# Kernel tuning notes

Hardware: AMD Instinct MI355X
Metric: run time of the kernel (lower is better)

Reference implementation:

```python
import jax, jax.numpy as jnp
import numpy as np

NEG_SLOPE = 0.2  # PyG HypergraphConv default negative_slope
HEADS, F_OUT = 4, 64


def setup_inputs() -> dict:
    key = jax.random.key(0)
    ks = jax.random.split(key, 8)
    N, E, NNZ, C_IN, C_OUT = 50000, 10000, 600000, 128, 64
    x = jax.random.normal(ks[0], (N, C_IN), jnp.float32)
    node = jax.random.randint(ks[1], (NNZ,), 0, N, jnp.int32)
    hedge = jax.random.randint(ks[2], (NNZ,), 0, E, jnp.int32)
    hedge = hedge.at[0].set(E - 1)  # ensure num_edges = max(hedge)+1 = E
    edge_index = jnp.stack([node, hedge])  # [2, NNZ]
    hyperedge_attr = jax.random.normal(ks[3], (E, C_IN), jnp.float32)  # init_hedge='rand'
    W1 = jax.random.normal(ks[4], (C_IN, HEADS * F_OUT), jnp.float32) / np.sqrt(C_IN)
    att1 = jax.random.normal(ks[5], (1, HEADS, 2 * F_OUT), jnp.float32) * 0.1
    b1 = jnp.zeros((HEADS * F_OUT,), jnp.float32)
    W2 = jax.random.normal(ks[6], (HEADS * F_OUT, C_OUT), jnp.float32) / np.sqrt(HEADS * F_OUT)
    b2 = jnp.zeros((C_OUT,), jnp.float32)
    return {"x": x, "edge_index": edge_index, "hyperedge_attr": hyperedge_attr,
            "W1": W1, "att1": att1, "b1": b1, "W2": W2, "b2": b2}


def _segment_softmax(logits, seg, num_segments):
    # PyG softmax: subtract per-segment max, exp, normalize with +1e-16
    m = jax.ops.segment_max(logits, seg, num_segments=num_segments)
    m = jnp.where(jnp.isfinite(m), m, 0.0)
    ex = jnp.exp(logits - m[seg])
    s = jax.ops.segment_sum(ex, seg, num_segments=num_segments)
    return ex / (s[seg] + 1e-16)


def _hconv(x, node, hedge, W, b, heads, f_out, num_edges, att=None, hyperedge_attr=None):
    """Faithful PyG HypergraphConv (attention_mode='node', concat=True)."""
    N = x.shape[0]
    E = num_edges
    nnz = node.shape[0]
    xh = (x @ W).reshape(N, heads, f_out)  # lin (bias-free) + view
    alpha = None
    if att is not None:
        he = (hyperedge_attr @ W).reshape(E, heads, f_out)
        # cat([x_i, x_j], -1) * att summed == split att into two halves
        alpha = (xh[node] * att[:, :, :f_out]).sum(-1) + (he[hedge] * att[:, :, f_out:]).sum(-1)
        alpha = jax.nn.leaky_relu(alpha, NEG_SLOPE)
        alpha = _segment_softmax(alpha, hedge, E)  # softmax per hyperedge ('node' mode)
    ones = jnp.ones((nnz,), x.dtype)
    D = jax.ops.segment_sum(ones, node, num_segments=N)  # node degrees (unit hyperedge weights)
    D = jnp.where(D > 0, 1.0 / D, 0.0)
    B = jax.ops.segment_sum(ones, hedge, num_segments=E)  # hyperedge sizes
    B = jnp.where(B > 0, 1.0 / B, 0.0)
    # propagate 1: nodes -> hyperedges (norm = B at target hyperedge)
    msg = B[hedge][:, None, None] * xh[node]
    if alpha is not None:
        msg = alpha[:, :, None] * msg
    eh = jax.ops.segment_sum(msg, hedge, num_segments=E)  # [E, H, F]
    # propagate 2: hyperedges -> nodes (norm = D at target node)
    msg2 = D[node][:, None, None] * eh[hedge]
    if alpha is not None:
        msg2 = alpha[:, :, None] * msg2
    out = jax.ops.segment_sum(msg2, node, num_segments=N)  # [N, H, F]
    return out.reshape(N, heads * f_out) + b


def reference(x, edge_index, hyperedge_attr, W1, att1, b1, W2, b2):
    node, hedge = edge_index[0], edge_index[1]
    E = hyperedge_attr.shape[0]  # num_edges = max(edge_index[1]) + 1 by construction
    h = _hconv(x, node, hedge, W1, b1, HEADS, F_OUT, E, att=att1, hyperedge_attr=hyperedge_attr)
    h = jax.nn.elu(h)  # dropout p=0 / eval mode -> identity
    out = _hconv(h, node, hedge, W2, b2, 1, W2.shape[1], E)  # last conv: no attention, heads=1
    return out
```

## Files before the change

### kernel.cpp

```cpp
#include <hip/hip_runtime.h>
#include <math.h>

#define LRELU_SLOPE 0.2f

static __device__ __forceinline__ float lrelu(float x) {
  return x >= 0.f ? x : LRELU_SLOPE * x;
}


__global__ void count_kernel(const int* __restrict__ node, const int* __restrict__ hedge,
                             int nnz, int* __restrict__ cnt_n, int* __restrict__ cnt_e) {
  int i = blockIdx.x * blockDim.x + threadIdx.x;
  if (i < nnz) {
    atomicAdd(&cnt_n[node[i]], 1);
    atomicAdd(&cnt_e[hedge[i]], 1);
  }
}

__global__ void recip_kernel(const int* __restrict__ cnt, float* __restrict__ rec, int n) {
  int i = blockIdx.x * blockDim.x + threadIdx.x;
  if (i < n) { int c = cnt[i]; rec[i] = c > 0 ? 1.f / (float)c : 0.f; }
}

__global__ __launch_bounds__(256) void scan1_kernel(const int* __restrict__ cnt,
                                                    int* __restrict__ off,
                                                    int* __restrict__ bsum, int n) {
  int b = blockIdx.x, tid = threadIdx.x, lane = tid & 63, wid = tid >> 6;
  int i0 = b * 1024 + tid * 4;
  int v0 = (i0 + 0 < n) ? cnt[i0 + 0] : 0;
  int v1 = (i0 + 1 < n) ? cnt[i0 + 1] : 0;
  int v2 = (i0 + 2 < n) ? cnt[i0 + 2] : 0;
  int v3 = (i0 + 3 < n) ? cnt[i0 + 3] : 0;
  int s = v0 + v1 + v2 + v3;
  int incl = s;
  #pragma unroll
  for (int d = 1; d < 64; d <<= 1) {
    int t = __shfl_up(incl, d);
    if (lane >= d) incl += t;
  }
  __shared__ int ws[4];
  if (lane == 63) ws[wid] = incl;
  __syncthreads();
  int woff = 0;
  #pragma unroll
  for (int w = 0; w < 4; ++w)
    if (w < wid) woff += ws[w];
  int run = woff + incl - s;
  if (i0 + 0 < n) off[i0 + 0] = run; run += v0;
  if (i0 + 1 < n) off[i0 + 1] = run; run += v1;
  if (i0 + 2 < n) off[i0 + 2] = run; run += v2;
  if (i0 + 3 < n) off[i0 + 3] = run;
  if (tid == 0) bsum[b] = ws[0] + ws[1] + ws[2] + ws[3];
}

__global__ void scan2_kernel(int* __restrict__ bsum, int nb) {
  int tid = threadIdx.x;
  int v = (tid < nb) ? bsum[tid] : 0;
  int incl = v;
  #pragma unroll
  for (int d = 1; d < 64; d <<= 1) {
    int t = __shfl_up(incl, d);
    if (tid >= d) incl += t;
  }
  if (tid < nb) bsum[tid] = incl - v;
  if (tid == 63) bsum[64] = incl;
}

__global__ void scan3_kernel(int* __restrict__ off, const int* __restrict__ bsum,
                             int n, int* __restrict__ cur) {
  int i = blockIdx.x * blockDim.x + threadIdx.x;
  if (i < n) {
    int v = off[i] + bsum[i >> 10];
    off[i] = v;
    cur[i] = v;
  }
  if (i == n) off[n] = bsum[64];
}

__global__ void scatter_kernel(const int* __restrict__ node, const int* __restrict__ hedge,
                               int nnz, int* __restrict__ cur_n, int* __restrict__ cur_e,
                               int* __restrict__ n_hedge, int* __restrict__ e_node) {
  int i = blockIdx.x * blockDim.x + threadIdx.x;
  if (i < nnz) {
    int nd = node[i], he = hedge[i];
    e_node[atomicAdd(&cur_e[he], 1)] = nd;
    n_hedge[atomicAdd(&cur_n[nd], 1)] = he;
  }
}


__global__ __launch_bounds__(256) void gemm1_kernel(
    const float* __restrict__ X, const float* __restrict__ W,
    float* __restrict__ Y, int R,
    const float* __restrict__ att, int half, float* __restrict__ adot) {
  __shared__ float xt[32][128];
  int r0 = blockIdx.x * 32;
  int tid = threadIdx.x, lane = tid & 63;
  int c0 = tid & 127, rh = tid >> 7;
  for (int i = tid; i < 32 * 32; i += 256) {
    int r = i >> 5, k4 = i & 31;
    int rr = r0 + r;
    float4 v = make_float4(0.f, 0.f, 0.f, 0.f);
    if (rr < R) v = reinterpret_cast<const float4*>(X)[(size_t)rr * 32 + k4];
    reinterpret_cast<float4*>(&xt[r][0])[k4] = v;
  }
  __syncthreads();
  float accA[16], accB[16];
  #pragma unroll
  for (int r = 0; r < 16; ++r) { accA[r] = 0.f; accB[r] = 0.f; }
  for (int k = 0; k < 128; k += 4) {
    float4 xv[16];
    #pragma unroll
    for (int r = 0; r < 16; ++r)
      xv[r] = *reinterpret_cast<const float4*>(&xt[rh * 16 + r][k]);
    #pragma unroll
    for (int kk = 0; kk < 4; ++kk) {
      float wa = W[(k + kk) * 256 + c0];
      float wb = W[(k + kk) * 256 + c0 + 128];
      #pragma unroll
      for (int r = 0; r < 16; ++r) {
        float xr = (kk == 0) ? xv[r].x : (kk == 1) ? xv[r].y : (kk == 2) ? xv[r].z : xv[r].w;
        accA[r] = fmaf(xr, wa, accA[r]);
        accB[r] = fmaf(xr, wb, accB[r]);
      }
    }
  }
  if (Y != nullptr) {
    #pragma unroll
    for (int r = 0; r < 16; ++r) {
      int rr = r0 + rh * 16 + r;
      if (rr < R) {
        Y[(size_t)rr * 256 + c0] = accA[r];
        Y[(size_t)rr * 256 + c0 + 128] = accB[r];
      }
    }
  }
  int hA = c0 >> 6;
  float avA = att[hA * 128 + half + lane];
  float avB = att[(hA + 2) * 128 + half + lane];
  #pragma unroll
  for (int r = 0; r < 16; ++r) {
    int rr = r0 + rh * 16 + r;
    float pA = accA[r] * avA;
    float pB = accB[r] * avB;
    #pragma unroll
    for (int s = 32; s >= 1; s >>= 1) {
      pA += __shfl_xor(pA, s);
      pB += __shfl_xor(pB, s);
    }
    if (lane == 0 && rr < R) {
      adot[rr * 4 + hA] = pA;
      adot[rr * 4 + hA + 2] = pB;
    }
  }
}


__global__ __launch_bounds__(256) void gemm2_kernel(const float* __restrict__ H,
                                                    const float* __restrict__ W,
                                                    float* __restrict__ Y, int R) {
  __shared__ float xt[32][256];
  int r0 = blockIdx.x * 32;
  int tid = threadIdx.x, c = tid & 63, rq = tid >> 6;
  for (int i = tid; i < 32 * 64; i += 256) {
    int r = i >> 6, k4 = i & 63;
    int rr = r0 + r;
    float4 v = make_float4(0.f, 0.f, 0.f, 0.f);
    if (rr < R) v = reinterpret_cast<const float4*>(H)[(size_t)rr * 64 + k4];
    reinterpret_cast<float4*>(&xt[r][0])[k4] = v;
  }
  __syncthreads();
  float acc[8];
  #pragma unroll
  for (int r = 0; r < 8; ++r) acc[r] = 0.f;
  for (int k = 0; k < 256; k += 4) {
    float4 xv[8];
    #pragma unroll
    for (int r = 0; r < 8; ++r)
      xv[r] = *reinterpret_cast<const float4*>(&xt[rq * 8 + r][k]);
    #pragma unroll
    for (int kk = 0; kk < 4; ++kk) {
      float w = W[(k + kk) * 64 + c];
      #pragma unroll
      for (int r = 0; r < 8; ++r) {
        float xr = (kk == 0) ? xv[r].x : (kk == 1) ? xv[r].y : (kk == 2) ? xv[r].z : xv[r].w;
        acc[r] = fmaf(xr, w, acc[r]);
      }
    }
  }
  #pragma unroll
  for (int r = 0; r < 8; ++r) {
    int rr = r0 + rq * 8 + r;
    if (rr < R) Y[(size_t)rr * 64 + c] = acc[r];
  }
}


__global__ __launch_bounds__(256) void p1_kernel(
    const int* __restrict__ off_e, const int* __restrict__ e_node,
    const float* __restrict__ xh, const float* __restrict__ a_n,
    const float* __restrict__ a_e, const float* __restrict__ Brec,
    float* __restrict__ eh, float4* __restrict__ pk, int E) {
  int tid = threadIdx.x, lane = tid & 63, wid = tid >> 6;
  int e = blockIdx.x * 4 + wid;
  if (e >= E) return;
  int beg = off_e[e], end = off_e[e + 1];
  int mm = lane & 15, h = lane >> 4, hsel = lane & 48;
  float aeh = a_e[e * 4 + h];

  float mx = -INFINITY;
  for (int base = beg; base < end; base += 16) {
    int m = base + mm;
    if (m < end) mx = fmaxf(mx, lrelu(a_n[e_node[m] * 4 + h] + aeh));
  }
  mx = fmaxf(mx, __shfl_xor(mx, 1));
  mx = fmaxf(mx, __shfl_xor(mx, 2));
  mx = fmaxf(mx, __shfl_xor(mx, 4));
  mx = fmaxf(mx, __shfl_xor(mx, 8));
  if (isinf(mx)) mx = 0.f;

  float4 acc = make_float4(0.f, 0.f, 0.f, 0.f);
  float ls = 0.f;
  for (int base = beg; base < end; base += 16) {
    int m = base + mm;
    int nd = 0;
    float w = 0.f;
    if (m < end) {
      nd = e_node[m];
      w = expf(lrelu(a_n[nd * 4 + h] + aeh) - mx);
      ls += w;
    }
    int cmax = min(16, end - base);
    for (int j = 0; j < cmax; ++j) {
      int ndj = __shfl(nd, j);
      float wj = __shfl(w, j | hsel);
      float4 v = reinterpret_cast<const float4*>(xh)[(size_t)ndj * 64 + lane];
      acc.x = fmaf(wj, v.x, acc.x);
      acc.y = fmaf(wj, v.y, acc.y);
      acc.z = fmaf(wj, v.z, acc.z);
      acc.w = fmaf(wj, v.w, acc.w);
    }
  }
  ls += __shfl_xor(ls, 1);
  ls += __shfl_xor(ls, 2);
  ls += __shfl_xor(ls, 4);
  ls += __shfl_xor(ls, 8);
  float rds = 1.f / (ls + 1e-16f);
  float sc = Brec[e] * rds;
  float4 o = make_float4(acc.x * sc, acc.y * sc, acc.z * sc, acc.w * sc);
  reinterpret_cast<float4*>(eh)[(size_t)e * 64 + lane] = o;
  if (mm == 0) pk[e * 4 + h] = make_float4(aeh, mx, rds, 0.f);
}

__global__ __launch_bounds__(256) void p2_kernel(
    const int* __restrict__ off_n, const int* __restrict__ n_hedge,
    const float* __restrict__ eh, const float* __restrict__ a_n,
    const float4* __restrict__ pk, const float* __restrict__ Drec,
    const float* __restrict__ b1, float* __restrict__ hout, int N) {
  int tid = threadIdx.x, lane = tid & 63, wid = tid >> 6;
  int n = blockIdx.x * 4 + wid;
  if (n >= N) return;
  int beg = off_n[n], end = off_n[n + 1];
  int mm = lane & 15, h = lane >> 4, hsel = lane & 48;
  float anh = a_n[n * 4 + h];

  float4 acc = make_float4(0.f, 0.f, 0.f, 0.f);
  for (int base = beg; base < end; base += 16) {
    int m = base + mm;
    int he = 0;
    float w = 0.f;
    if (m < end) {
      he = n_hedge[m];
      float4 p = pk[he * 4 + h];
      w = expf(lrelu(anh + p.x) - p.y) * p.z;
    }
    int cmax = min(16, end - base);
    for (int j = 0; j < cmax; ++j) {
      int hej = __shfl(he, j);
      float wj = __shfl(w, j | hsel);
      float4 v = reinterpret_cast<const float4*>(eh)[(size_t)hej * 64 + lane];
      acc.x = fmaf(wj, v.x, acc.x);
      acc.y = fmaf(wj, v.y, acc.y);
      acc.z = fmaf(wj, v.z, acc.z);
      acc.w = fmaf(wj, v.w, acc.w);
    }
  }
  float dr = Drec[n];
  float4 bb = reinterpret_cast<const float4*>(b1)[lane];
  float vx = fmaf(acc.x, dr, bb.x);
  float vy = fmaf(acc.y, dr, bb.y);
  float vz = fmaf(acc.z, dr, bb.z);
  float vw = fmaf(acc.w, dr, bb.w);
  float4 o;
  o.x = vx > 0.f ? vx : expm1f(vx);
  o.y = vy > 0.f ? vy : expm1f(vy);
  o.z = vz > 0.f ? vz : expm1f(vz);
  o.w = vw > 0.f ? vw : expm1f(vw);
  reinterpret_cast<float4*>(hout)[(size_t)n * 64 + lane] = o;
}


__global__ __launch_bounds__(256) void p1b_kernel(
    const int* __restrict__ off_e, const int* __restrict__ e_node,
    const float* __restrict__ xh2, const float* __restrict__ Brec,
    float* __restrict__ eh2, int E) {
  int tid = threadIdx.x, lane = tid & 63, wid = tid >> 6;
  int e = blockIdx.x * 4 + wid;
  if (e >= E) return;
  int f4 = lane & 15, mo = lane >> 4;
  int beg = off_e[e], end = off_e[e + 1];
  float4 acc = make_float4(0.f, 0.f, 0.f, 0.f);
  for (int m = beg + mo; m < end; m += 4) {
    float4 v = reinterpret_cast<const float4*>(xh2)[(size_t)e_node[m] * 16 + f4];
    acc.x += v.x; acc.y += v.y; acc.z += v.z; acc.w += v.w;
  }
  acc.x += __shfl_xor(acc.x, 16); acc.x += __shfl_xor(acc.x, 32);
  acc.y += __shfl_xor(acc.y, 16); acc.y += __shfl_xor(acc.y, 32);
  acc.z += __shfl_xor(acc.z, 16); acc.z += __shfl_xor(acc.z, 32);
  acc.w += __shfl_xor(acc.w, 16); acc.w += __shfl_xor(acc.w, 32);
  if (mo == 0) {
    float sc = Brec[e];
    float4 o = make_float4(acc.x * sc, acc.y * sc, acc.z * sc, acc.w * sc);
    reinterpret_cast<float4*>(eh2)[(size_t)e * 16 + f4] = o;
  }
}

__global__ __launch_bounds__(256) void p2b_kernel(
    const int* __restrict__ off_n, const int* __restrict__ n_hedge,
    const float* __restrict__ eh2, const float* __restrict__ Drec,
    const float* __restrict__ b2, float* __restrict__ out, int N) {
  int tid = threadIdx.x, lane = tid & 63, wid = tid >> 6;
  int n = blockIdx.x * 4 + wid;
  if (n >= N) return;
  int f4 = lane & 15, mo = lane >> 4;
  int beg = off_n[n], end = off_n[n + 1];
  float4 acc = make_float4(0.f, 0.f, 0.f, 0.f);
  for (int m = beg + mo; m < end; m += 4) {
    float4 v = reinterpret_cast<const float4*>(eh2)[(size_t)n_hedge[m] * 16 + f4];
    acc.x += v.x; acc.y += v.y; acc.z += v.z; acc.w += v.w;
  }
  acc.x += __shfl_xor(acc.x, 16); acc.x += __shfl_xor(acc.x, 32);
  acc.y += __shfl_xor(acc.y, 16); acc.y += __shfl_xor(acc.y, 32);
  acc.z += __shfl_xor(acc.z, 16); acc.z += __shfl_xor(acc.z, 32);
  acc.w += __shfl_xor(acc.w, 16); acc.w += __shfl_xor(acc.w, 32);
  if (mo == 0) {
    float dr = Drec[n];
    float4 bb = reinterpret_cast<const float4*>(b2)[f4];
    float4 o = make_float4(fmaf(acc.x, dr, bb.x), fmaf(acc.y, dr, bb.y),
                           fmaf(acc.z, dr, bb.z), fmaf(acc.w, dr, bb.w));
    reinterpret_cast<float4*>(out)[(size_t)n * 16 + f4] = o;
  }
}


extern "C" void kernel_launch(void* const* d_in, const int* in_sizes, int n_in,
                              void* d_out, int out_size, void* d_ws, size_t ws_size,
                              hipStream_t stream) {
  const float* x   = (const float*)d_in[0];
  const int*   ei  = (const int*)d_in[1];
  const float* hea = (const float*)d_in[2];
  const float* W1  = (const float*)d_in[3];
  const float* att = (const float*)d_in[4];
  const float* b1  = (const float*)d_in[5];
  const float* W2  = (const float*)d_in[6];
  const float* b2  = (const float*)d_in[7];

  const int C2  = in_sizes[7];
  const int CH  = in_sizes[6] / C2;
  const int CIN = in_sizes[3] / CH;
  const int N   = in_sizes[0] / CIN;
  const int E   = in_sizes[2] / CIN;
  const int NNZ = in_sizes[1] / 2;
  const int* node  = ei;
  const int* hedge = ei + NNZ;

  char* wp = (char*)d_ws;
  auto alloc = [&](size_t bytes) -> void* {
    void* p = (void*)wp;
    wp += (bytes + 255) & ~(size_t)255;
    return p;
  };
  float*  xh     = (float*) alloc((size_t)N * CH * 4);
  float*  eh     = (float*) alloc((size_t)E * CH * 4);
  float*  a_n    = (float*) alloc((size_t)N * 4 * 4);
  float*  a_e    = (float*) alloc((size_t)E * 4 * 4);
  float4* pk     = (float4*)alloc((size_t)E * 4 * 16);
  float*  Brec   = (float*) alloc((size_t)E * 4);
  float*  Drec   = (float*) alloc((size_t)N * 4);
  int*    cnt_e  = (int*)   alloc((size_t)E * 4);
  int*    cnt_n  = (int*)   alloc((size_t)N * 4);
  int*    off_e  = (int*)   alloc((size_t)(E + 1) * 4);
  int*    off_n  = (int*)   alloc((size_t)(N + 1) * 4);
  int*    cur_e  = (int*)   alloc((size_t)E * 4);
  int*    cur_n  = (int*)   alloc((size_t)N * 4);
  int*    e_node  = (int*)  alloc((size_t)NNZ * 4);
  int*    n_hedge = (int*)  alloc((size_t)NNZ * 4);
  float*  xh2    = (float*) alloc((size_t)N * C2 * 4);
  float*  eh2    = (float*) alloc((size_t)E * C2 * 4);
  int*    bsum_e = (int*)   alloc(65 * 4);
  int*    bsum_n = (int*)   alloc(65 * 4);
  float*  hact   = xh;

  hipMemsetAsync(cnt_e, 0, (size_t)E * 4, stream);
  hipMemsetAsync(cnt_n, 0, (size_t)N * 4, stream);

  const int tpb = 256;
  count_kernel<<<(NNZ + tpb - 1) / tpb, tpb, 0, stream>>>(node, hedge, NNZ, cnt_n, cnt_e);

  int nbE = (E + 1023) / 1024, nbN = (N + 1023) / 1024;
  scan1_kernel<<<nbE, 256, 0, stream>>>(cnt_e, off_e, bsum_e, E);
  scan2_kernel<<<1, 64, 0, stream>>>(bsum_e, nbE);
  scan3_kernel<<<(E + 1 + 255) / 256, 256, 0, stream>>>(off_e, bsum_e, E, cur_e);
  scan1_kernel<<<nbN, 256, 0, stream>>>(cnt_n, off_n, bsum_n, N);
  scan2_kernel<<<1, 64, 0, stream>>>(bsum_n, nbN);
  scan3_kernel<<<(N + 1 + 255) / 256, 256, 0, stream>>>(off_n, bsum_n, N, cur_n);

  recip_kernel<<<(E + tpb - 1) / tpb, tpb, 0, stream>>>(cnt_e, Brec, E);
  recip_kernel<<<(N + tpb - 1) / tpb, tpb, 0, stream>>>(cnt_n, Drec, N);
  scatter_kernel<<<(NNZ + tpb - 1) / tpb, tpb, 0, stream>>>(node, hedge, NNZ,
                                                            cur_n, cur_e, n_hedge, e_node);

  gemm1_kernel<<<(N + 31) / 32, 256, 0, stream>>>(x, W1, xh, N, att, 0, a_n);
  gemm1_kernel<<<(E + 31) / 32, 256, 0, stream>>>(hea, W1, nullptr, E, att, 64, a_e);

  p1_kernel<<<(E + 3) / 4, 256, 0, stream>>>(off_e, e_node, xh, a_n, a_e, Brec, eh, pk, E);
  p2_kernel<<<(N + 3) / 4, 256, 0, stream>>>(off_n, n_hedge, eh, a_n, pk, Drec, b1, hact, N);

  gemm2_kernel<<<(N + 31) / 32, 256, 0, stream>>>(hact, W2, xh2, N);
  p1b_kernel<<<(E + 3) / 4, 256, 0, stream>>>(off_e, e_node, xh2, Brec, eh2, E);
  p2b_kernel<<<(N + 3) / 4, 256, 0, stream>>>(off_n, n_hedge, eh2, Drec, b2, (float*)d_out, N);
}
```

Measured before the change: 603.9 us.

## Store intermediate features in bf16 and precompute per-incidence attention weights

Node and hyperedge feature intermediates (xh, eh, hact, xh2) are now packed as bf16 pairs instead of fp32, roughly halving gather traffic in the propagation kernels. The scatter kernel records each incidence's position in the node-major order, so p1 can write unnormalized attention weights into a per-incidence buffer. The softmax normalization is folded into eh, and p2 then reads alpha directly instead of recomputing exp per edge. The gather loops are restructured to load 8 rows at a time with two accumulators, and the small recip and scan2 launches are merged. This trades fp32 accuracy for bandwidth and adds an NNZ*4 float alpha buffer plus the npos array.

```diff
diff --git a/kernel.cpp b/kernel.cpp
--- a/kernel.cpp
+++ b/kernel.cpp
@@ -1,10 +1,24 @@
 #include <hip/hip_runtime.h>
 #include <math.h>
 
+typedef unsigned int u32;
+
 #define LRELU_SLOPE 0.2f
 
 static __device__ __forceinline__ float lrelu(float x) {
   return x >= 0.f ? x : LRELU_SLOPE * x;
+}
+static __device__ __forceinline__ float bflo(u32 u) {
+  return __builtin_bit_cast(float, u << 16);
+}
+static __device__ __forceinline__ float bfhi(u32 u) {
+  return __builtin_bit_cast(float, u & 0xFFFF0000u);
+}
+static __device__ __forceinline__ u32 f2bf_pack(float a, float b) {
+  u32 ua = __builtin_bit_cast(u32, a), ub = __builtin_bit_cast(u32, b);
+  ua = (ua + 0x7FFFu + ((ua >> 16) & 1u)) >> 16;
+  ub = (ub + 0x7FFFu + ((ub >> 16) & 1u)) & 0xFFFF0000u;
+  return ua | ub;
 }
 
 
@@ -17,20 +31,20 @@
   }
 }
 
-__global__ void recip_kernel(const int* __restrict__ cnt, float* __restrict__ rec, int n) {
-  int i = blockIdx.x * blockDim.x + threadIdx.x;
-  if (i < n) { int c = cnt[i]; rec[i] = c > 0 ? 1.f / (float)c : 0.f; }
-}
-
 __global__ __launch_bounds__(256) void scan1_kernel(const int* __restrict__ cnt,
                                                     int* __restrict__ off,
-                                                    int* __restrict__ bsum, int n) {
+                                                    int* __restrict__ bsum,
+                                                    float* __restrict__ rec, int n) {
   int b = blockIdx.x, tid = threadIdx.x, lane = tid & 63, wid = tid >> 6;
   int i0 = b * 1024 + tid * 4;
   int v0 = (i0 + 0 < n) ? cnt[i0 + 0] : 0;
   int v1 = (i0 + 1 < n) ? cnt[i0 + 1] : 0;
   int v2 = (i0 + 2 < n) ? cnt[i0 + 2] : 0;
   int v3 = (i0 + 3 < n) ? cnt[i0 + 3] : 0;
+  if (i0 + 0 < n) rec[i0 + 0] = v0 > 0 ? 1.f / (float)v0 : 0.f;
+  if (i0 + 1 < n) rec[i0 + 1] = v1 > 0 ? 1.f / (float)v1 : 0.f;
+  if (i0 + 2 < n) rec[i0 + 2] = v2 > 0 ? 1.f / (float)v2 : 0.f;
+  if (i0 + 3 < n) rec[i0 + 3] = v3 > 0 ? 1.f / (float)v3 : 0.f;
   int s = v0 + v1 + v2 + v3;
   int incl = s;
   #pragma unroll
@@ -53,17 +67,20 @@
   if (tid == 0) bsum[b] = ws[0] + ws[1] + ws[2] + ws[3];
 }
 
-__global__ void scan2_kernel(int* __restrict__ bsum, int nb) {
+__global__ void scan2_kernel(int* __restrict__ bsum_e, int nbe,
+                             int* __restrict__ bsum_n, int nbn) {
+  int* b = blockIdx.x == 0 ? bsum_e : bsum_n;
+  int nb = blockIdx.x == 0 ? nbe : nbn;
   int tid = threadIdx.x;
-  int v = (tid < nb) ? bsum[tid] : 0;
+  int v = (tid < nb) ? b[tid] : 0;
   int incl = v;
   #pragma unroll
   for (int d = 1; d < 64; d <<= 1) {
     int t = __shfl_up(incl, d);
     if (tid >= d) incl += t;
   }
-  if (tid < nb) bsum[tid] = incl - v;
-  if (tid == 63) bsum[64] = incl;
+  if (tid < nb) b[tid] = incl - v;
+  if (tid == 63) b[64] = incl;
 }
 
 __global__ void scan3_kernel(int* __restrict__ off, const int* __restrict__ bsum,
@@ -79,29 +96,32 @@
 
 __global__ void scatter_kernel(const int* __restrict__ node, const int* __restrict__ hedge,
                                int nnz, int* __restrict__ cur_n, int* __restrict__ cur_e,
-                               int* __restrict__ n_hedge, int* __restrict__ e_node) {
+                               int* __restrict__ n_hedge, int* __restrict__ e_node,
+                               int* __restrict__ npos) {
   int i = blockIdx.x * blockDim.x + threadIdx.x;
   if (i < nnz) {
     int nd = node[i], he = hedge[i];
-    e_node[atomicAdd(&cur_e[he], 1)] = nd;
-    n_hedge[atomicAdd(&cur_n[nd], 1)] = he;
+    int pe = atomicAdd(&cur_e[he], 1);
+    int pn = atomicAdd(&cur_n[nd], 1);
+    e_node[pe] = nd;
+    n_hedge[pn] = he;
+    npos[pe] = pn;
   }
 }
 
 
 __global__ __launch_bounds__(256) void gemm1_kernel(
     const float* __restrict__ X, const float* __restrict__ W,
-    float* __restrict__ Y, int R,
+    u32* __restrict__ Yb, int R,
     const float* __restrict__ att, int half, float* __restrict__ adot) {
   __shared__ float xt[32][128];
-  int r0 = blockIdx.x * 32;
-  int tid = threadIdx.x, lane = tid & 63;
-  int c0 = tid & 127, rh = tid >> 7;
+  int r0 = blockIdx.x * 32, tid = threadIdx.x, lane = tid & 63;
+  int c = tid & 127, rh = tid >> 7;
   for (int i = tid; i < 32 * 32; i += 256) {
     int r = i >> 5, k4 = i & 31;
     int rr = r0 + r;
-    float4 v = make_float4(0.f, 0.f, 0.f, 0.f);
-    if (rr < R) v = reinterpret_cast<const float4*>(X)[(size_t)rr * 32 + k4];
+    float4 v = rr < R ? reinterpret_cast<const float4*>(X)[(size_t)rr * 32 + k4]
+                      : make_float4(0.f, 0.f, 0.f, 0.f);
     reinterpret_cast<float4*>(&xt[r][0])[k4] = v;
   }
   __syncthreads();
@@ -115,8 +135,8 @@
       xv[r] = *reinterpret_cast<const float4*>(&xt[rh * 16 + r][k]);
     #pragma unroll
     for (int kk = 0; kk < 4; ++kk) {
-      float wa = W[(k + kk) * 256 + c0];
-      float wb = W[(k + kk) * 256 + c0 + 128];
+      float wa = W[(k + kk) * 256 + 2 * c];
+      float wb = W[(k + kk) * 256 + 2 * c + 1];
       #pragma unroll
       for (int r = 0; r < 16; ++r) {
         float xr = (kk == 0) ? xv[r].x : (kk == 1) ? xv[r].y : (kk == 2) ? xv[r].z : xv[r].w;
@@ -125,203 +145,274 @@
       }
     }
   }
-  if (Y != nullptr) {
+  if (Yb != nullptr) {
     #pragma unroll
     for (int r = 0; r < 16; ++r) {
       int rr = r0 + rh * 16 + r;
-      if (rr < R) {
-        Y[(size_t)rr * 256 + c0] = accA[r];
-        Y[(size_t)rr * 256 + c0 + 128] = accB[r];
-      }
-    }
-  }
-  int hA = c0 >> 6;
-  float avA = att[hA * 128 + half + lane];
-  float avB = att[(hA + 2) * 128 + half + lane];
+      if (rr < R) Yb[(size_t)rr * 128 + c] = f2bf_pack(accA[r], accB[r]);
+    }
+  }
+  int hh = c >> 5, cl = c & 31;
+  float avA = att[hh * 128 + half + 2 * cl];
+  float avB = att[hh * 128 + half + 2 * cl + 1];
   #pragma unroll
   for (int r = 0; r < 16; ++r) {
+    float p = fmaf(accA[r], avA, accB[r] * avB);
+    #pragma unroll
+    for (int s = 16; s >= 1; s >>= 1) p += __shfl_xor(p, s);
     int rr = r0 + rh * 16 + r;
-    float pA = accA[r] * avA;
-    float pB = accB[r] * avB;
-    #pragma unroll
-    for (int s = 32; s >= 1; s >>= 1) {
-      pA += __shfl_xor(pA, s);
-      pB += __shfl_xor(pB, s);
-    }
-    if (lane == 0 && rr < R) {
-      adot[rr * 4 + hA] = pA;
-      adot[rr * 4 + hA + 2] = pB;
-    }
-  }
-}
-
-
-__global__ __launch_bounds__(256) void gemm2_kernel(const float* __restrict__ H,
-                                                    const float* __restrict__ W,
-                                                    float* __restrict__ Y, int R) {
-  __shared__ float xt[32][256];
-  int r0 = blockIdx.x * 32;
-  int tid = threadIdx.x, c = tid & 63, rq = tid >> 6;
-  for (int i = tid; i < 32 * 64; i += 256) {
-    int r = i >> 6, k4 = i & 63;
+    if ((lane & 31) == 0 && rr < R) adot[rr * 4 + hh] = p;
+  }
+}
+
+
+__global__ __launch_bounds__(256) void gemm2_kernel(
+    const u32* __restrict__ Hb, const float* __restrict__ W,
+    u32* __restrict__ Yb, int R) {
+  __shared__ u32 ht[32][128];
+  int r0 = blockIdx.x * 32, tid = threadIdx.x;
+  int cp = tid & 31, rg = tid >> 5;
+  for (int i = tid; i < 32 * 32; i += 256) {
+    int r = i >> 5, q = i & 31;
     int rr = r0 + r;
-    float4 v = make_float4(0.f, 0.f, 0.f, 0.f);
-    if (rr < R) v = reinterpret_cast<const float4*>(H)[(size_t)rr * 64 + k4];
-    reinterpret_cast<float4*>(&xt[r][0])[k4] = v;
+    uint4 v = rr < R ? reinterpret_cast<const uint4*>(Hb)[(size_t)rr * 32 + q]
+                     : make_uint4(0u, 0u, 0u, 0u);
+    reinterpret_cast<uint4*>(&ht[r][0])[q] = v;
   }
   __syncthreads();
-  float acc[8];
+  float acc[4][2] = {};
+  for (int k = 0; k < 256; k += 4) {
+    float w0a = W[(k + 0) * 64 + 2 * cp], w0b = W[(k + 0) * 64 + 2 * cp + 1];
+    float w1a = W[(k + 1) * 64 + 2 * cp], w1b = W[(k + 1) * 64 + 2 * cp + 1];
+    float w2a = W[(k + 2) * 64 + 2 * cp], w2b = W[(k + 2) * 64 + 2 * cp + 1];
+    float w3a = W[(k + 3) * 64 + 2 * cp], w3b = W[(k + 3) * 64 + 2 * cp + 1];
+    #pragma unroll
+    for (int r = 0; r < 4; ++r) {
+      uint2 u = *reinterpret_cast<const uint2*>(&ht[rg * 4 + r][k >> 1]);
+      float x0 = bflo(u.x), x1 = bfhi(u.x), x2 = bflo(u.y), x3 = bfhi(u.y);
+      acc[r][0] = fmaf(x0, w0a, acc[r][0]); acc[r][1] = fmaf(x0, w0b, acc[r][1]);
+      acc[r][0] = fmaf(x1, w1a, acc[r][0]); acc[r][1] = fmaf(x1, w1b, acc[r][1]);
+      acc[r][0] = fmaf(x2, w2a, acc[r][0]); acc[r][1] = fmaf(x2, w2b, acc[r][1]);
+      acc[r][0] = fmaf(x3, w3a, acc[r][0]); acc[r][1] = fmaf(x3, w3b, acc[r][1]);
+    }
+  }
   #pragma unroll
-  for (int r = 0; r < 8; ++r) acc[r] = 0.f;
-  for (int k = 0; k < 256; k += 4) {
-    float4 xv[8];
-    #pragma unroll
-    for (int r = 0; r < 8; ++r)
-      xv[r] = *reinterpret_cast<const float4*>(&xt[rq * 8 + r][k]);
-    #pragma unroll
-    for (int kk = 0; kk < 4; ++kk) {
-      float w = W[(k + kk) * 64 + c];
-      #pragma unroll
-      for (int r = 0; r < 8; ++r) {
-        float xr = (kk == 0) ? xv[r].x : (kk == 1) ? xv[r].y : (kk == 2) ? xv[r].z : xv[r].w;
-        acc[r] = fmaf(xr, w, acc[r]);
-      }
-    }
-  }
-  #pragma unroll
-  for (int r = 0; r < 8; ++r) {
-    int rr = r0 + rq * 8 + r;
-    if (rr < R) Y[(size_t)rr * 64 + c] = acc[r];
+  for (int r = 0; r < 4; ++r) {
+    int rr = r0 + rg * 4 + r;
+    if (rr < R) Yb[(size_t)rr * 32 + cp] = f2bf_pack(acc[r][0], acc[r][1]);
   }
 }
 
 
 __global__ __launch_bounds__(256) void p1_kernel(
     const int* __restrict__ off_e, const int* __restrict__ e_node,
-    const float* __restrict__ xh, const float* __restrict__ a_n,
-    const float* __restrict__ a_e, const float* __restrict__ Brec,
-    float* __restrict__ eh, float4* __restrict__ pk, int E) {
-  int tid = threadIdx.x, lane = tid & 63, wid = tid >> 6;
+    const int* __restrict__ npos, const u32* __restrict__ xhb,
+    const float* __restrict__ a_n, const float* __restrict__ a_e,
+    const float* __restrict__ Brec, float* __restrict__ alpha_n,
+    u32* __restrict__ ehb, int E) {
+  int tid = threadIdx.x, lane = tid & 63;
+  int wid = __builtin_amdgcn_readfirstlane(tid >> 6);
   int e = blockIdx.x * 4 + wid;
   if (e >= E) return;
   int beg = off_e[e], end = off_e[e + 1];
-  int mm = lane & 15, h = lane >> 4, hsel = lane & 48;
+  int h = lane >> 4;
+  bool h0 = (lane & 15) == 0;
   float aeh = a_e[e * 4 + h];
 
   float mx = -INFINITY;
-  for (int base = beg; base < end; base += 16) {
-    int m = base + mm;
-    if (m < end) mx = fmaxf(mx, lrelu(a_n[e_node[m] * 4 + h] + aeh));
-  }
-  mx = fmaxf(mx, __shfl_xor(mx, 1));
-  mx = fmaxf(mx, __shfl_xor(mx, 2));
-  mx = fmaxf(mx, __shfl_xor(mx, 4));
-  mx = fmaxf(mx, __shfl_xor(mx, 8));
+  {
+    int m = beg;
+    for (; m + 8 <= end; m += 8) {
+      float l[8];
+      #pragma unroll
+      for (int i = 0; i < 8; ++i) {
+        int nd = e_node[m + i];
+        l[i] = lrelu(a_n[nd * 4 + h] + aeh);
+      }
+      #pragma unroll
+      for (int i = 0; i < 8; ++i) mx = fmaxf(mx, l[i]);
+    }
+    if (m < end) {
+      int last = end - 1;
+      #pragma unroll
+      for (int i = 0; i < 8; ++i) {
+        int mm = m + i, mc = mm < last ? mm : last;
+        int nd = e_node[mc];
+        mx = fmaxf(mx, lrelu(a_n[nd * 4 + h] + aeh));
+      }
+    }
+  }
   if (isinf(mx)) mx = 0.f;
 
-  float4 acc = make_float4(0.f, 0.f, 0.f, 0.f);
+  const uint2* rows = reinterpret_cast<const uint2*>(xhb);
+  float4 A = make_float4(0.f, 0.f, 0.f, 0.f), B = A;
   float ls = 0.f;
-  for (int base = beg; base < end; base += 16) {
-    int m = base + mm;
-    int nd = 0;
-    float w = 0.f;
-    if (m < end) {
-      nd = e_node[m];
-      w = expf(lrelu(a_n[nd * 4 + h] + aeh) - mx);
-      ls += w;
-    }
-    int cmax = min(16, end - base);
-    for (int j = 0; j < cmax; ++j) {
-      int ndj = __shfl(nd, j);
-      float wj = __shfl(w, j | hsel);
-      float4 v = reinterpret_cast<const float4*>(xh)[(size_t)ndj * 64 + lane];
-      acc.x = fmaf(wj, v.x, acc.x);
-      acc.y = fmaf(wj, v.y, acc.y);
-      acc.z = fmaf(wj, v.z, acc.z);
-      acc.w = fmaf(wj, v.w, acc.w);
-    }
-  }
-  ls += __shfl_xor(ls, 1);
-  ls += __shfl_xor(ls, 2);
-  ls += __shfl_xor(ls, 4);
-  ls += __shfl_xor(ls, 8);
+  int m = beg;
+  for (; m + 8 <= end; m += 8) {
+    int ns[8]; float wsv[8];
+    #pragma unroll
+    for (int i = 0; i < 8; ++i) {
+      ns[i] = e_node[m + i];
+      wsv[i] = expf(lrelu(a_n[ns[i] * 4 + h] + aeh) - mx);
+      ls += wsv[i];
+      if (h0) alpha_n[npos[m + i] * 4 + h] = wsv[i];
+    }
+    uint2 vs[8];
+    #pragma unroll
+    for (int i = 0; i < 8; ++i) vs[i] = rows[(size_t)ns[i] * 64 + lane];
+    #pragma unroll
+    for (int i = 0; i < 8; ++i) {
+      float4& C = (i & 1) ? B : A;
+      C.x = fmaf(wsv[i], bflo(vs[i].x), C.x);
+      C.y = fmaf(wsv[i], bfhi(vs[i].x), C.y);
+      C.z = fmaf(wsv[i], bflo(vs[i].y), C.z);
+      C.w = fmaf(wsv[i], bfhi(vs[i].y), C.w);
+    }
+  }
+  if (m < end) {
+    int last = end - 1;
+    int ns[8]; float wsv[8];
+    #pragma unroll
+    for (int i = 0; i < 8; ++i) {
+      int mm = m + i, mc = mm < last ? mm : last;
+      ns[i] = e_node[mc];
+      float w = expf(lrelu(a_n[ns[i] * 4 + h] + aeh) - mx);
+      bool v = mm < end;
+      wsv[i] = v ? w : 0.f;
+      ls += wsv[i];
+      if (v && h0) alpha_n[npos[mc] * 4 + h] = w;
+    }
+    uint2 vs[8];
+    #pragma unroll
+    for (int i = 0; i < 8; ++i) vs[i] = rows[(size_t)ns[i] * 64 + lane];
+    #pragma unroll
+    for (int i = 0; i < 8; ++i) {
+      float4& C = (i & 1) ? B : A;
+      C.x = fmaf(wsv[i], bflo(vs[i].x), C.x);
+      C.y = fmaf(wsv[i], bfhi(vs[i].x), C.y);
+      C.z = fmaf(wsv[i], bflo(vs[i].y), C.z);
+      C.w = fmaf(wsv[i], bfhi(vs[i].y), C.w);
+    }
+  }
   float rds = 1.f / (ls + 1e-16f);
-  float sc = Brec[e] * rds;
-  float4 o = make_float4(acc.x * sc, acc.y * sc, acc.z * sc, acc.w * sc);
-  reinterpret_cast<float4*>(eh)[(size_t)e * 64 + lane] = o;
-  if (mm == 0) pk[e * 4 + h] = make_float4(aeh, mx, rds, 0.f);
-}
+  float sc = (Brec[e] * rds) * rds;
+  uint2 st;
+  st.x = f2bf_pack((A.x + B.x) * sc, (A.y + B.y) * sc);
+  st.y = f2bf_pack((A.z + B.z) * sc, (A.w + B.w) * sc);
+  reinterpret_cast<uint2*>(ehb)[(size_t)e * 64 + lane] = st;
+}
+
 
 __global__ __launch_bounds__(256) void p2_kernel(
     const int* __restrict__ off_n, const int* __restrict__ n_hedge,
-    const float* __restrict__ eh, const float* __restrict__ a_n,
-    const float4* __restrict__ pk, const float* __restrict__ Drec,
-    const float* __restrict__ b1, float* __restrict__ hout, int N) {
-  int tid = threadIdx.x, lane = tid & 63, wid = tid >> 6;
+    const u32* __restrict__ ehb, const float* __restrict__ alpha_n,
+    const float* __restrict__ Drec, const float* __restrict__ b1,
+    u32* __restrict__ hactb, int N) {
+  int tid = threadIdx.x, lane = tid & 63;
+  int wid = __builtin_amdgcn_readfirstlane(tid >> 6);
   int n = blockIdx.x * 4 + wid;
   if (n >= N) return;
   int beg = off_n[n], end = off_n[n + 1];
-  int mm = lane & 15, h = lane >> 4, hsel = lane & 48;
-  float anh = a_n[n * 4 + h];
-
-  float4 acc = make_float4(0.f, 0.f, 0.f, 0.f);
-  for (int base = beg; base < end; base += 16) {
-    int m = base + mm;
-    int he = 0;
-    float w = 0.f;
-    if (m < end) {
-      he = n_hedge[m];
-      float4 p = pk[he * 4 + h];
-      w = expf(lrelu(anh + p.x) - p.y) * p.z;
-    }
-    int cmax = min(16, end - base);
-    for (int j = 0; j < cmax; ++j) {
-      int hej = __shfl(he, j);
-      float wj = __shfl(w, j | hsel);
-      float4 v = reinterpret_cast<const float4*>(eh)[(size_t)hej * 64 + lane];
-      acc.x = fmaf(wj, v.x, acc.x);
-      acc.y = fmaf(wj, v.y, acc.y);
-      acc.z = fmaf(wj, v.z, acc.z);
-      acc.w = fmaf(wj, v.w, acc.w);
+  int h = lane >> 4;
+  const uint2* rows = reinterpret_cast<const uint2*>(ehb);
+  float4 A = make_float4(0.f, 0.f, 0.f, 0.f), B = A;
+  int m = beg;
+  for (; m + 8 <= end; m += 8) {
+    int es[8]; float wsv[8];
+    #pragma unroll
+    for (int i = 0; i < 8; ++i) {
+      es[i] = n_hedge[m + i];
+      wsv[i] = alpha_n[(m + i) * 4 + h];
+    }
+    uint2 vs[8];
+    #pragma unroll
+    for (int i = 0; i < 8; ++i) vs[i] = rows[(size_t)es[i] * 64 + lane];
+    #pragma unroll
+    for (int i = 0; i < 8; ++i) {
+      float4& C = (i & 1) ? B : A;
+      C.x = fmaf(wsv[i], bflo(vs[i].x), C.x);
+      C.y = fmaf(wsv[i], bfhi(vs[i].x), C.y);
+      C.z = fmaf(wsv[i], bflo(vs[i].y), C.z);
+      C.w = fmaf(wsv[i], bfhi(vs[i].y), C.w);
+    }
+  }
+  if (m < end) {
+    int last = end - 1;
+    int es[8]; float wsv[8];
+    #pragma unroll
+    for (int i = 0; i < 8; ++i) {
+      int mm = m + i, mc = mm < last ? mm : last;
+      es[i] = n_hedge[mc];
+      wsv[i] = (mm < end) ? alpha_n[mc * 4 + h] : 0.f;
+    }
+    uint2 vs[8];
+    #pragma unroll
+    for (int i = 0; i < 8; ++i) vs[i] = rows[(size_t)es[i] * 64 + lane];
+    #pragma unroll
+    for (int i = 0; i < 8; ++i) {
+      float4& C = (i & 1) ? B : A;
+      C.x = fmaf(wsv[i], bflo(vs[i].x), C.x);
+      C.y = fmaf(wsv[i], bfhi(vs[i].x), C.y);
+      C.z = fmaf(wsv[i], bflo(vs[i].y), C.z);
+      C.w = fmaf(wsv[i], bfhi(vs[i].y), C.w);
     }
   }
   float dr = Drec[n];
   float4 bb = reinterpret_cast<const float4*>(b1)[lane];
-  float vx = fmaf(acc.x, dr, bb.x);
-  float vy = fmaf(acc.y, dr, bb.y);
-  float vz = fmaf(acc.z, dr, bb.z);
-  float vw = fmaf(acc.w, dr, bb.w);
-  float4 o;
-  o.x = vx > 0.f ? vx : expm1f(vx);
-  o.y = vy > 0.f ? vy : expm1f(vy);
-  o.z = vz > 0.f ? vz : expm1f(vz);
-  o.w = vw > 0.f ? vw : expm1f(vw);
-  reinterpret_cast<float4*>(hout)[(size_t)n * 64 + lane] = o;
+  float vx = fmaf(A.x + B.x, dr, bb.x);
+  float vy = fmaf(A.y + B.y, dr, bb.y);
+  float vz = fmaf(A.z + B.z, dr, bb.z);
+  float vw = fmaf(A.w + B.w, dr, bb.w);
+  vx = vx > 0.f ? vx : expm1f(vx);
+  vy = vy > 0.f ? vy : expm1f(vy);
+  vz = vz > 0.f ? vz : expm1f(vz);
+  vw = vw > 0.f ? vw : expm1f(vw);
+  uint2 st;
+  st.x = f2bf_pack(vx, vy);
+  st.y = f2bf_pack(vz, vw);
+  reinterpret_cast<uint2*>(hactb)[(size_t)n * 64 + lane] = st;
 }
 
 
 __global__ __launch_bounds__(256) void p1b_kernel(
     const int* __restrict__ off_e, const int* __restrict__ e_node,
-    const float* __restrict__ xh2, const float* __restrict__ Brec,
+    const u32* __restrict__ xh2b, const float* __restrict__ Brec,
     float* __restrict__ eh2, int E) {
-  int tid = threadIdx.x, lane = tid & 63, wid = tid >> 6;
+  int tid = threadIdx.x, lane = tid & 63;
+  int wid = __builtin_amdgcn_readfirstlane(tid >> 6);
   int e = blockIdx.x * 4 + wid;
   if (e >= E) return;
-  int f4 = lane & 15, mo = lane >> 4;
+  int f8 = lane & 15, mo = lane >> 4;
   int beg = off_e[e], end = off_e[e + 1];
-  float4 acc = make_float4(0.f, 0.f, 0.f, 0.f);
-  for (int m = beg + mo; m < end; m += 4) {
-    float4 v = reinterpret_cast<const float4*>(xh2)[(size_t)e_node[m] * 16 + f4];
-    acc.x += v.x; acc.y += v.y; acc.z += v.z; acc.w += v.w;
-  }
-  acc.x += __shfl_xor(acc.x, 16); acc.x += __shfl_xor(acc.x, 32);
-  acc.y += __shfl_xor(acc.y, 16); acc.y += __shfl_xor(acc.y, 32);
-  acc.z += __shfl_xor(acc.z, 16); acc.z += __shfl_xor(acc.z, 32);
-  acc.w += __shfl_xor(acc.w, 16); acc.w += __shfl_xor(acc.w, 32);
+  const uint2* rows = reinterpret_cast<const uint2*>(xh2b);
+  float4 A = make_float4(0.f, 0.f, 0.f, 0.f), B = A;
+  int m = beg;
+  for (; m + 8 <= end; m += 8) {
+    int n0 = e_node[m + mo], n1 = e_node[m + 4 + mo];
+    uint2 u0 = rows[(size_t)n0 * 16 + f8];
+    uint2 u1 = rows[(size_t)n1 * 16 + f8];
+    A.x += bflo(u0.x); A.y += bfhi(u0.x); A.z += bflo(u0.y); A.w += bfhi(u0.y);
+    B.x += bflo(u1.x); B.y += bfhi(u1.x); B.z += bflo(u1.y); B.w += bfhi(u1.y);
+  }
+  if (m < end) {
+    int last = end - 1;
+    int mm0 = m + mo, mm1 = m + 4 + mo;
+    int mc0 = mm0 < last ? mm0 : last, mc1 = mm1 < last ? mm1 : last;
+    int n0 = e_node[mc0], n1 = e_node[mc1];
+    uint2 u0 = rows[(size_t)n0 * 16 + f8];
+    uint2 u1 = rows[(size_t)n1 * 16 + f8];
+    if (mm0 < end) { A.x += bflo(u0.x); A.y += bfhi(u0.x); A.z += bflo(u0.y); A.w += bfhi(u0.y); }
+    if (mm1 < end) { B.x += bflo(u1.x); B.y += bfhi(u1.x); B.z += bflo(u1.y); B.w += bfhi(u1.y); }
+  }
+  A.x += B.x; A.y += B.y; A.z += B.z; A.w += B.w;
+  A.x += __shfl_xor(A.x, 16); A.x += __shfl_xor(A.x, 32);
+  A.y += __shfl_xor(A.y, 16); A.y += __shfl_xor(A.y, 32);
+  A.z += __shfl_xor(A.z, 16); A.z += __shfl_xor(A.z, 32);
+  A.w += __shfl_xor(A.w, 16); A.w += __shfl_xor(A.w, 32);
   if (mo == 0) {
     float sc = Brec[e];
-    float4 o = make_float4(acc.x * sc, acc.y * sc, acc.z * sc, acc.w * sc);
-    reinterpret_cast<float4*>(eh2)[(size_t)e * 16 + f4] = o;
+    float4 o = make_float4(A.x * sc, A.y * sc, A.z * sc, A.w * sc);
+    reinterpret_cast<float4*>(eh2)[(size_t)e * 16 + f8] = o;
   }
 }
 
@@ -329,26 +420,43 @@
     const int* __restrict__ off_n, const int* __restrict__ n_hedge,
     const float* __restrict__ eh2, const float* __restrict__ Drec,
     const float* __restrict__ b2, float* __restrict__ out, int N) {
-  int tid = threadIdx.x, lane = tid & 63, wid = tid >> 6;
+  int tid = threadIdx.x, lane = tid & 63;
+  int wid = __builtin_amdgcn_readfirstlane(tid >> 6);
   int n = blockIdx.x * 4 + wid;
   if (n >= N) return;
-  int f4 = lane & 15, mo = lane >> 4;
+  int f8 = lane & 15, mo = lane >> 4;
   int beg = off_n[n], end = off_n[n + 1];
-  float4 acc = make_float4(0.f, 0.f, 0.f, 0.f);
-  for (int m = beg + mo; m < end; m += 4) {
-    float4 v = reinterpret_cast<const float4*>(eh2)[(size_t)n_hedge[m] * 16 + f4];
-    acc.x += v.x; acc.y += v.y; acc.z += v.z; acc.w += v.w;
-  }
-  acc.x += __shfl_xor(acc.x, 16); acc.x += __shfl_xor(acc.x, 32);
-  acc.y += __shfl_xor(acc.y, 16); acc.y += __shfl_xor(acc.y, 32);
-  acc.z += __shfl_xor(acc.z, 16); acc.z += __shfl_xor(acc.z, 32);
-  acc.w += __shfl_xor(acc.w, 16); acc.w += __shfl_xor(acc.w, 32);
+  const float4* rows = reinterpret_cast<const float4*>(eh2);
+  float4 A = make_float4(0.f, 0.f, 0.f, 0.f), B = A;
+  int m = beg;
+  for (; m + 8 <= end; m += 8) {
+    int e0 = n_hedge[m + mo], e1 = n_hedge[m + 4 + mo];
+    float4 v0 = rows[(size_t)e0 * 16 + f8];
+    float4 v1 = rows[(size_t)e1 * 16 + f8];
+    A.x += v0.x; A.y += v0.y; A.z += v0.z; A.w += v0.w;
+    B.x += v1.x; B.y += v1.y; B.z += v1.z; B.w += v1.w;
+  }
+  if (m < end) {
+    int last = end - 1;
+    int mm0 = m + mo, mm1 = m + 4 + mo;
+    int mc0 = mm0 < last ? mm0 : last, mc1 = mm1 < last ? mm1 : last;
+    int e0 = n_hedge[mc0], e1 = n_hedge[mc1];
+    float4 v0 = rows[(size_t)e0 * 16 + f8];
+    float4 v1 = rows[(size_t)e1 * 16 + f8];
+    if (mm0 < end) { A.x += v0.x; A.y += v0.y; A.z += v0.z; A.w += v0.w; }
+    if (mm1 < end) { B.x += v1.x; B.y += v1.y; B.z += v1.z; B.w += v1.w; }
+  }
+  A.x += B.x; A.y += B.y; A.z += B.z; A.w += B.w;
+  A.x += __shfl_xor(A.x, 16); A.x += __shfl_xor(A.x, 32);
+  A.y += __shfl_xor(A.y, 16); A.y += __shfl_xor(A.y, 32);
+  A.z += __shfl_xor(A.z, 16); A.z += __shfl_xor(A.z, 32);
+  A.w += __shfl_xor(A.w, 16); A.w += __shfl_xor(A.w, 32);
   if (mo == 0) {
     float dr = Drec[n];
-    float4 bb = reinterpret_cast<const float4*>(b2)[f4];
-    float4 o = make_float4(fmaf(acc.x, dr, bb.x), fmaf(acc.y, dr, bb.y),
-                           fmaf(acc.z, dr, bb.z), fmaf(acc.w, dr, bb.w));
-    reinterpret_cast<float4*>(out)[(size_t)n * 16 + f4] = o;
+    float4 bb = reinterpret_cast<const float4*>(b2)[f8];
+    float4 o = make_float4(fmaf(A.x, dr, bb.x), fmaf(A.y, dr, bb.y),
+                           fmaf(A.z, dr, bb.z), fmaf(A.w, dr, bb.w));
+    reinterpret_cast<float4*>(out)[(size_t)n * 16 + f8] = o;
   }
 }
 
@@ -380,26 +488,27 @@
     wp += (bytes + 255) & ~(size_t)255;
     return p;
   };
-  float*  xh     = (float*) alloc((size_t)N * CH * 4);
-  float*  eh     = (float*) alloc((size_t)E * CH * 4);
-  float*  a_n    = (float*) alloc((size_t)N * 4 * 4);
-  float*  a_e    = (float*) alloc((size_t)E * 4 * 4);
-  float4* pk     = (float4*)alloc((size_t)E * 4 * 16);
-  float*  Brec   = (float*) alloc((size_t)E * 4);
-  float*  Drec   = (float*) alloc((size_t)N * 4);
-  int*    cnt_e  = (int*)   alloc((size_t)E * 4);
-  int*    cnt_n  = (int*)   alloc((size_t)N * 4);
-  int*    off_e  = (int*)   alloc((size_t)(E + 1) * 4);
-  int*    off_n  = (int*)   alloc((size_t)(N + 1) * 4);
-  int*    cur_e  = (int*)   alloc((size_t)E * 4);
-  int*    cur_n  = (int*)   alloc((size_t)N * 4);
-  int*    e_node  = (int*)  alloc((size_t)NNZ * 4);
-  int*    n_hedge = (int*)  alloc((size_t)NNZ * 4);
-  float*  xh2    = (float*) alloc((size_t)N * C2 * 4);
-  float*  eh2    = (float*) alloc((size_t)E * C2 * 4);
-  int*    bsum_e = (int*)   alloc(65 * 4);
-  int*    bsum_n = (int*)   alloc(65 * 4);
-  float*  hact   = xh;
+  u32*   xhb     = (u32*)  alloc((size_t)N * (CH / 2) * 4);
+  u32*   ehb     = (u32*)  alloc((size_t)E * (CH / 2) * 4);
+  u32*   hactb   = (u32*)  alloc((size_t)N * (CH / 2) * 4);
+  u32*   xh2b    = (u32*)  alloc((size_t)N * (C2 / 2) * 4);
+  float* eh2     = (float*)alloc((size_t)E * C2 * 4);
+  float* a_n     = (float*)alloc((size_t)N * 4 * 4);
+  float* a_e     = (float*)alloc((size_t)E * 4 * 4);
+  float* alpha_n = (float*)alloc((size_t)NNZ * 4 * 4);
+  float* Brec    = (float*)alloc((size_t)E * 4);
+  float* Drec    = (float*)alloc((size_t)N * 4);
+  int*   cnt_e   = (int*)  alloc((size_t)E * 4);
+  int*   cnt_n   = (int*)  alloc((size_t)N * 4);
+  int*   off_e   = (int*)  alloc((size_t)(E + 1) * 4);
+  int*   off_n   = (int*)  alloc((size_t)(N + 1) * 4);
+  int*   cur_e   = (int*)  alloc((size_t)E * 4);
+  int*   cur_n   = (int*)  alloc((size_t)N * 4);
+  int*   e_node  = (int*)  alloc((size_t)NNZ * 4);
+  int*   n_hedge = (int*)  alloc((size_t)NNZ * 4);
+  int*   npos    = (int*)  alloc((size_t)NNZ * 4);
+  int*   bsum_e  = (int*)  alloc(65 * 4);
+  int*   bsum_n  = (int*)  alloc(65 * 4);
 
   hipMemsetAsync(cnt_e, 0, (size_t)E * 4, stream);
   hipMemsetAsync(cnt_n, 0, (size_t)N * 4, stream);
@@ -408,25 +517,25 @@
   count_kernel<<<(NNZ + tpb - 1) / tpb, tpb, 0, stream>>>(node, hedge, NNZ, cnt_n, cnt_e);
 
   int nbE = (E + 1023) / 1024, nbN = (N + 1023) / 1024;
-  scan1_kernel<<<nbE, 256, 0, stream>>>(cnt_e, off_e, bsum_e, E);
-  scan2_kernel<<<1, 64, 0, stream>>>(bsum_e, nbE);
+  scan1_kernel<<<nbE, 256, 0, stream>>>(cnt_e, off_e, bsum_e, Brec, E);
+  scan1_kernel<<<nbN, 256, 0, stream>>>(cnt_n, off_n, bsum_n, Drec, N);
+  scan2_kernel<<<2, 64, 0, stream>>>(bsum_e, nbE, bsum_n, nbN);
   scan3_kernel<<<(E + 1 + 255) / 256, 256, 0, stream>>>(off_e, bsum_e, E, cur_e);
-  scan1_kernel<<<nbN, 256, 0, stream>>>(cnt_n, off_n, bsum_n, N);
-  scan2_kernel<<<1, 64, 0, stream>>>(bsum_n, nbN);
   scan3_kernel<<<(N + 1 + 255) / 256, 256, 0, stream>>>(off_n, bsum_n, N, cur_n);
 
-  recip_kernel<<<(E + tpb - 1) / tpb, tpb, 0, stream>>>(cnt_e, Brec, E);
-  recip_kernel<<<(N + tpb - 1) / tpb, tpb, 0, stream>>>(cnt_n, Drec, N);
-  scatter_kernel<<<(NNZ + tpb - 1) / tpb, tpb, 0, stream>>>(node, hedge, NNZ,
-                                                            cur_n, cur_e, n_hedge, e_node);
-
-  gemm1_kernel<<<(N + 31) / 32, 256, 0, stream>>>(x, W1, xh, N, att, 0, a_n);
+  scatter_kernel<<<(NNZ + tpb - 1) / tpb, tpb, 0, stream>>>(
+      node, hedge, NNZ, cur_n, cur_e, n_hedge, e_node, npos);
+
+  gemm1_kernel<<<(N + 31) / 32, 256, 0, stream>>>(x, W1, xhb, N, att, 0, a_n);
   gemm1_kernel<<<(E + 31) / 32, 256, 0, stream>>>(hea, W1, nullptr, E, att, 64, a_e);
 
-  p1_kernel<<<(E + 3) / 4, 256, 0, stream>>>(off_e, e_node, xh, a_n, a_e, Brec, eh, pk, E);
-  p2_kernel<<<(N + 3) / 4, 256, 0, stream>>>(off_n, n_hedge, eh, a_n, pk, Drec, b1, hact, N);
-
-  gemm2_kernel<<<(N + 31) / 32, 256, 0, stream>>>(hact, W2, xh2, N);
-  p1b_kernel<<<(E + 3) / 4, 256, 0, stream>>>(off_e, e_node, xh2, Brec, eh2, E);
-  p2b_kernel<<<(N + 3) / 4, 256, 0, stream>>>(off_n, n_hedge, eh2, Drec, b2, (float*)d_out, N);
-}
+  p1_kernel<<<(E + 3) / 4, 256, 0, stream>>>(off_e, e_node, npos, xhb, a_n, a_e,
+                                             Brec, alpha_n, ehb, E);
+  p2_kernel<<<(N + 3) / 4, 256, 0, stream>>>(off_n, n_hedge, ehb, alpha_n,
+                                             Drec, b1, hactb, N);
+
+  gemm2_kernel<<<(N + 31) / 32, 256, 0, stream>>>(hactb, W2, xh2b, N);
+  p1b_kernel<<<(E + 3) / 4, 256, 0, stream>>>(off_e, e_node, xh2b, Brec, eh2, E);
+  p2b_kernel<<<(N + 3) / 4, 256, 0, stream>>>(off_n, n_hedge, eh2, Drec, b2,
+                                              (float*)d_out, N);
+}
```

Result: faster. 543.1 us (-10.1%).
